# Performance work log

Hardware: AMD Instinct MI355X
Metric: run time of the kernel (lower is better)

Reference implementation:

```python
import jax, jax.numpy as jnp
import numpy as np

B, L, D_MODEL, N_HEADS = 2, 2048, 1024, 16
HEAD_DIM = D_MODEL // N_HEADS  # 64
PAD_START = (3 * L) // 4  # last quarter of keys are padding


def _rope_tables(seq_len, dim, base=10000.0, dtype=jnp.float32):
    inv_freq = 1.0 / (base ** (jnp.arange(0, dim, 2, dtype=jnp.float32) / dim))
    t = jnp.arange(seq_len, dtype=jnp.float32)
    freqs = jnp.einsum('i,j->ij', t, inv_freq)  # (L, dim/2)
    return jnp.cos(freqs).astype(dtype), jnp.sin(freqs).astype(dtype)


def _apply_rope(x, cos, sin):
    # x: (B, H, L, D); cos/sin: (L, D/2)
    cos = cos[None, None]
    sin = sin[None, None]
    x_even, x_odd = x[..., 0::2], x[..., 1::2]
    rot_even = x_even * cos - x_odd * sin
    rot_odd = x_even * sin + x_odd * cos
    return jnp.stack((rot_even, rot_odd), axis=-1).reshape(x.shape)


def setup_inputs() -> dict:
    key = jax.random.key(0)
    k_x, k_wqkv, k_bqkv, k_wout, k_bout = jax.random.split(key, 5)
    x = jax.random.normal(k_x, (B, L, D_MODEL), dtype=jnp.float32)
    Wqkv = jax.random.normal(k_wqkv, (3 * D_MODEL, D_MODEL), dtype=jnp.float32) * 0.02
    bqkv = jax.random.normal(k_bqkv, (3 * D_MODEL,), dtype=jnp.float32) * 0.02
    Wout = jax.random.normal(k_wout, (D_MODEL, D_MODEL), dtype=jnp.float32) * 0.02
    bout = jax.random.normal(k_bout, (D_MODEL,), dtype=jnp.float32) * 0.02
    # True = padded position (end of sequence padded)
    pad_mask = jnp.broadcast_to(jnp.arange(L) >= PAD_START, (B, L))
    return {"x": x, "pad_mask": pad_mask, "Wqkv": Wqkv, "bqkv": bqkv, "Wout": Wout, "bout": bout}


def reference(x, pad_mask, Wqkv, bqkv, Wout, bout):
    Bc, Lc, E = x.shape
    H, D = N_HEADS, HEAD_DIM
    qkv = x @ Wqkv.T + bqkv                       # (B, L, 3E)
    qkv = qkv.reshape(Bc, Lc, 3, H, D)
    q = jnp.transpose(qkv[:, :, 0], (0, 2, 1, 3))  # (B, H, L, D)
    k = jnp.transpose(qkv[:, :, 1], (0, 2, 1, 3))
    v = jnp.transpose(qkv[:, :, 2], (0, 2, 1, 3))
    cos, sin = _rope_tables(Lc, D, dtype=x.dtype)
    q = _apply_rope(q, cos, sin)
    k = _apply_rope(k, cos, sin)
    # Mask exactly as the torch module builds it: attn_mask = causal_upper | key_pad,
    # with torch bool-mask semantics (True = allowed to attend).
    causal_upper = jnp.triu(jnp.ones((Lc, Lc), dtype=bool), 1)[None, None]  # (1,1,L,L)
    key_pad = pad_mask[:, None, None, :]                                     # (B,1,1,L)
    allowed = causal_upper | key_pad                                         # (B,1,L,L)
    scale = 1.0 / jnp.sqrt(jnp.asarray(D, dtype=x.dtype))
    scores = jnp.einsum('bhqd,bhkd->bhqk', q, k) * scale
    scores = jnp.where(allowed, scores, -jnp.inf)
    attn = jax.nn.softmax(scores, axis=-1)
    out = jnp.einsum('bhqk,bhkd->bhqd', attn, v)   # (B, H, L, D)
    out = jnp.transpose(out, (0, 2, 1, 3)).reshape(Bc, Lc, E)
    return out @ Wout.T + bout
```

## Files before the change

kernel.cpp:

```cpp
#include <hip/hip_runtime.h>

#define BB 2
#define LL 2048
#define DM 1024
#define NH 16
#define HD 64
#define PAD_START 1536

typedef short bf16x8 __attribute__((ext_vector_type(8)));
typedef float f32x4 __attribute__((ext_vector_type(4)));

#define MFMA_B16(a, b, c) __builtin_amdgcn_mfma_f32_16x16x32_bf16(a, b, c, 0, 0, 0)

#define GLOAD_LDS16(g, l)                                            \
    __builtin_amdgcn_global_load_lds(                                \
        (const __attribute__((address_space(1))) void*)(g),          \
        (__attribute__((address_space(3))) void*)(l), 16, 0, 0)

__device__ __forceinline__ float bf2f(unsigned short u) {
    union { unsigned int i; float f; } v; v.i = ((unsigned int)u) << 16; return v.f;
}
__device__ __forceinline__ unsigned short f2bf(float f) {
    union { float f; unsigned int i; } v; v.f = f;
    unsigned int x = v.i;
    return (unsigned short)((x + 0x7fffu + ((x >> 16) & 1u)) >> 16);
}

__global__ __launch_bounds__(256) void split_kernel(
    const float* __restrict__ X, const float* __restrict__ Wq,
    const float* __restrict__ Wo,
    unsigned short* __restrict__ Xh,
    unsigned short* __restrict__ Wh,
    unsigned short* __restrict__ Woh,
    float* __restrict__ cosT, float* __restrict__ sinT)
{
    if (blockIdx.x >= 8192) {
        const int idx = (blockIdx.x - 8192) * 256 + threadIdx.x;
        const int l = idx >> 5, pp = idx & 31;
        const float LOG2_1E4 = 13.287712379549449f;
        const float invf = exp2f(-((float)pp) * (LOG2_1E4 / 32.0f));
        const float ang = (float)l * invf;
        float2 cs; cs.x = cosf(ang); cs.y = sinf(ang);
        ((float2*)cosT)[idx] = cs;
        return;
    }
    const size_t e = ((size_t)blockIdx.x * 256 + threadIdx.x) * 4;
    const float* src; unsigned short* dh; size_t o;
    if (e < 4194304)      { src = X;  dh = Xh;  o = e; }
    else if (e < 7340032) { src = Wq; dh = Wh;  o = e - 4194304; }
    else                  { src = Wo; dh = Woh; o = e - 7340032; }
    float4 v = *(const float4*)(src + o);
    ushort4 hv;
    hv.x = f2bf(v.x); hv.y = f2bf(v.y);
    hv.z = f2bf(v.z); hv.w = f2bf(v.w);
    *(ushort4*)(dh + o) = hv;
}

__device__ __forceinline__ void qk_frag(
    f32x4 cf, int r0, int bh, int d, float bv, float qscale,
    const float2* __restrict__ ct2,
    unsigned short* __restrict__ dst, bool odd)
{
    const int p = d >> 1;
#pragma unroll
    for (int e = 0; e < 4; ++e) {
        const int l = (r0 + e) & (LL - 1);
        const float x = cf[e] + bv;
        const float px = __shfl_xor(x, 1);
        const float2 cs = ct2[l * 32 + p];
        const float ve = odd ? px : x;
        const float vo = odd ? x : px;
        float res = odd ? (ve * cs.y + vo * cs.x) : (ve * cs.x - vo * cs.y);
        res *= qscale;
        const float other = __shfl_xor(res, 1);
        if (!odd) {
            const unsigned int pk = ((unsigned int)f2bf(res)) |
                                    (((unsigned int)f2bf(other)) << 16);
            *(unsigned int*)(dst + ((size_t)bh * LL + l) * HD + d) = pk;
        }
    }
}

__device__ __forceinline__ void v_frag(
    f32x4 cf, int l0, int bh, int d, float bv, unsigned short* __restrict__ vt)
{
    ushort4 pk;
    pk.x = f2bf(cf[0] + bv); pk.y = f2bf(cf[1] + bv);
    pk.z = f2bf(cf[2] + bv); pk.w = f2bf(cf[3] + bv);
    *(ushort4*)(vt + ((size_t)(bh * HD + d)) * LL + l0) = pk;
}

__device__ __forceinline__ void out_frag(
    f32x4 cf, int r0, int c, float bv, float* __restrict__ C)
{
#pragma unroll
    for (int e = 0; e < 4; ++e)
        C[(size_t)(r0 + e) * DM + c] = cf[e] + bv;
}

__global__ __launch_bounds__(512) void qkv_mfma(
    const unsigned short* __restrict__ Xh,
    const unsigned short* __restrict__ Wh,
    const float* __restrict__ bias,
    const float* __restrict__ cosT,
    unsigned short* __restrict__ qs, unsigned short* __restrict__ ks,
    unsigned short* __restrict__ vt)
{
    __shared__ unsigned short As[2 * 256 * 64];
    __shared__ unsigned short Bs[2 * 192 * 64];

    const int bid = blockIdx.y * 16 + blockIdx.x;
    const int xcd = bid & 7;
    const int i   = bid >> 3;
    const int mt  = (xcd & 3) * 4 + (i & 3);
    const int nt  = (xcd >> 2) * 8 + (i >> 2);
    const int m0 = mt * 256, n0 = nt * 192;

    const int t = threadIdx.x;
    const int lane = t & 63;
    const int w = t >> 6;
    const int wm = w >> 2;
    const int wn = w & 3;
    const int lm = lane & 15;
    const int quad = lane >> 4;

    const int rop = lane >> 3;
    const int sw  = ((lane & 7) ^ rop) * 8;
    const unsigned short* ga = Xh + (size_t)(m0 + w * 32 + rop) * 1024 + sw;
    const unsigned short* gb = Wh + (size_t)(n0 + w * 24 + rop) * 1024 + sw;
    unsigned short* lA = As + (w * 32) * 64;
    unsigned short* lB = Bs + (w * 24) * 64;

    const int o1 = (quad ^ (lm & 7)) * 8;
    const int o2 = ((quad + 4) ^ (lm & 7)) * 8;
    const int ar = (wm * 128 + lm) * 64;
    const int br = (wn * 48 + lm) * 64;

    f32x4 acc[8][3];
#pragma unroll
    for (int mf = 0; mf < 8; ++mf)
#pragma unroll
        for (int nf = 0; nf < 3; ++nf) acc[mf][nf] = (f32x4){0.f,0.f,0.f,0.f};

#define STG(ABO, BBO, k0)                                                 \
    do {                                                                  \
        GLOAD_LDS16(ga + (k0),             lA + (ABO));                   \
        GLOAD_LDS16(ga + (k0) +  8 * 1024, lA + (ABO) +  8 * 64);         \
        GLOAD_LDS16(ga + (k0) + 16 * 1024, lA + (ABO) + 16 * 64);         \
        GLOAD_LDS16(ga + (k0) + 24 * 1024, lA + (ABO) + 24 * 64);         \
        GLOAD_LDS16(gb + (k0),             lB + (BBO));                   \
        GLOAD_LDS16(gb + (k0) +  8 * 1024, lB + (BBO) +  8 * 64);         \
        GLOAD_LDS16(gb + (k0) + 16 * 1024, lB + (BBO) + 16 * 64);         \
    } while (0)

#define TILE(ABO, BBO, SG, KS, VMN)                                      \
    {                                                                     \
        bf16x8 af[8][2]; bf16x8 bfr[3][2];                                \
        _Pragma("unroll")                                                 \
        for (int mf = 0; mf < 8; ++mf) {                                  \
            af[mf][0] = *(const bf16x8*)(As + (ABO) + ar + mf * 1024 + o1);\
            af[mf][1] = *(const bf16x8*)(As + (ABO) + ar + mf * 1024 + o2);\
        }                                                                 \
        _Pragma("unroll")                                                 \
        for (int nf = 0; nf < 3; ++nf) {                                  \
            bfr[nf][0] = *(const bf16x8*)(Bs + (BBO) + br + nf * 1024 + o1);\
            bfr[nf][1] = *(const bf16x8*)(Bs + (BBO) + br + nf * 1024 + o2);\
        }                                                                 \
        asm volatile("s_waitcnt lgkmcnt(0)" ::: "memory");                \
        __builtin_amdgcn_sched_barrier(0);                                \
        __builtin_amdgcn_s_barrier();                                     \
        if (SG) { STG(ABO, BBO, KS); }      \
        asm volatile("s_waitcnt vmcnt(" VMN ")" ::: "memory");            \
        __builtin_amdgcn_sched_barrier(0);                                \
        __builtin_amdgcn_s_barrier();                                     \
        __builtin_amdgcn_s_setprio(1);                                    \
        _Pragma("unroll")                                                 \
        for (int mf = 0; mf < 8; ++mf) {                                  \
            _Pragma("unroll")                                             \
            for (int nf = 0; nf < 3; ++nf) {                              \
                acc[mf][nf] = MFMA_B16(af[mf][0], bfr[nf][0], acc[mf][nf]);\
                acc[mf][nf] = MFMA_B16(af[mf][1], bfr[nf][1], acc[mf][nf]);\
            }                                                             \
        }                                                                 \
        __builtin_amdgcn_s_setprio(0);                                    \
    }

    STG(0, 0, 0);
    STG(16384, 12288, 64);
    asm volatile("s_waitcnt vmcnt(7)" ::: "memory");
    __builtin_amdgcn_sched_barrier(0);
    __builtin_amdgcn_s_barrier();

    for (int k0 = 0; k0 < 896; k0 += 128) {
        TILE(0,     0,     1, k0 + 128, "7")
        TILE(16384, 12288, 1, k0 + 192, "7")
    }
    TILE(0,     0,     0, 0, "0")
    TILE(16384, 12288, 0, 0, "0")
#undef TILE
#undef STG

    const int bi = m0 >> 11;
    const int rbase = m0 + wm * 128;
    const int cbase = n0 + wn * 48;
    const bool odd = (lm & 1) != 0;
    const float2* ct2 = (const float2*)cosT;

#pragma unroll
    for (int nf = 0; nf < 3; ++nf) {
        const int col0 = cbase + nf * 16;
        const int s = col0 >> 10;
        const int h = (col0 & 1023) >> 6;
        const int bh = bi * NH + h;
        const int d = (col0 & 63) + lm;
        const float bv = bias[col0 + lm];
        if (s == 2) {
#pragma unroll
            for (int mf = 0; mf < 8; ++mf)
                v_frag(acc[mf][nf], (rbase + mf * 16 + quad * 4) & (LL - 1),
                       bh, d, bv, vt);
        } else {
            unsigned short* dst = (s == 0) ? qs : ks;
            const float qscale = (s == 0) ? 0.125f : 1.0f;
#pragma unroll
            for (int mf = 0; mf < 8; ++mf)
                qk_frag(acc[mf][nf], rbase + mf * 16 + quad * 4, bh,
                        d, bv, qscale, ct2, dst, odd);
        }
    }
}

__global__ __launch_bounds__(256) void attn_mfma(
    const unsigned short* __restrict__ qs,
    const unsigned short* __restrict__ ks,
    const unsigned short* __restrict__ vt,
    unsigned short* __restrict__ aoh)
{
    __shared__ unsigned short Ks[2][64 * 72];
    __shared__ unsigned short Vs[2][64 * 72];
    __shared__ unsigned short Pl[4][16 * 72];

    const int bh = blockIdx.y;
    const int qt = (blockIdx.x + blockIdx.y) & 31;
    const int q0 = qt * 64;
    const int b = bh >> 4, h = bh & (NH - 1);
    const int tid = threadIdx.x;
    const int w = tid >> 6;
    const int lane = tid & 63;
    const int lm = lane & 15;
    const int quad = lane >> 4;
    const int qw0 = q0 + w * 16;

    const unsigned short* qbase = qs + ((size_t)bh * LL + qw0 + lm) * HD + quad * 8;
    const bf16x8 qf0 = *(const bf16x8*)(qbase);
    const bf16x8 qf1 = *(const bf16x8*)(qbase + 32);

    f32x4 O[4];
#pragma unroll
    for (int dd = 0; dd < 4; ++dd) O[dd] = (f32x4){0.f, 0.f, 0.f, 0.f};
    float lrow[4] = {0.f, 0.f, 0.f, 0.f};

    const unsigned short* kbase = ks + (size_t)bh * LL * HD;
    const unsigned short* vtb   = vt + (size_t)bh * HD * LL;
    unsigned short* pw = &Pl[w][0];

    const int srow = tid >> 3;
    const int sch  = (tid & 7) * 8;

    const int t0 = ((q0 < PAD_START) ? q0 : PAD_START) >> 6;

    int k0 = t0 * 64;
    uint4 ka0 = *(const uint4*)(kbase + (size_t)(k0 + srow) * HD + sch);
    uint4 ka1 = *(const uint4*)(kbase + (size_t)(k0 + srow + 32) * HD + sch);
    uint4 va0 = *(const uint4*)(vtb + (size_t)srow * LL + k0 + sch);
    uint4 va1 = *(const uint4*)(vtb + (size_t)(srow + 32) * LL + k0 + sch);
    {
        unsigned short* Kc = &Ks[t0 & 1][0];
        unsigned short* Vc = &Vs[t0 & 1][0];
        *(uint4*)(Kc + srow * 72 + sch)        = ka0;
        *(uint4*)(Kc + (srow + 32) * 72 + sch) = ka1;
        *(uint4*)(Vc + srow * 72 + sch)        = va0;
        *(uint4*)(Vc + (srow + 32) * 72 + sch) = va1;
    }
    __syncthreads();

    for (int tt = t0; tt < 32; ++tt) {
        k0 = tt * 64;
        const int cur = tt & 1;
        const unsigned short* Kc = &Ks[cur][0];
        const unsigned short* Vc = &Vs[cur][0];
        unsigned short* Kn = &Ks[cur ^ 1][0];
        unsigned short* Vn = &Vs[cur ^ 1][0];

        {
            const int kn = ((tt + 1) < 32 ? (tt + 1) : 31) * 64;
            ka0 = *(const uint4*)(kbase + (size_t)(kn + srow) * HD + sch);
            ka1 = *(const uint4*)(kbase + (size_t)(kn + srow + 32) * HD + sch);
            va0 = *(const uint4*)(vtb + (size_t)srow * LL + kn + sch);
            va1 = *(const uint4*)(vtb + (size_t)(srow + 32) * LL + kn + sch);
        }

        f32x4 sfrag[4];
#pragma unroll
        for (int c = 0; c < 4; ++c) {
            const bf16x8 kf0 = *(const bf16x8*)(Kc + (c * 16 + lm) * 72 + quad * 8);
            const bf16x8 kf1 = *(const bf16x8*)(Kc + (c * 16 + lm) * 72 + 32 + quad * 8);
            f32x4 z = (f32x4){0.f, 0.f, 0.f, 0.f};
            z = MFMA_B16(qf0, kf0, z);
            z = MFMA_B16(qf1, kf1, z);
            sfrag[c] = z;
        }
        if (tt == t0 && q0 < PAD_START) {
#pragma unroll
            for (int c = 0; c < 4; ++c) {
                const int kg = k0 + c * 16 + lm;
#pragma unroll
                for (int r = 0; r < 4; ++r) {
                    const int qg = qw0 + quad * 4 + r;
                    if (kg <= qg) sfrag[c][r] = -1e30f;
                }
            }
        }
#pragma unroll
        for (int r = 0; r < 4; ++r) {
#pragma unroll
            for (int c = 0; c < 4; ++c) {
                const float p = __expf(sfrag[c][r]);
                lrow[r] += p;
                pw[(quad * 4 + r) * 72 + c * 16 + lm] = f2bf(p);
            }
        }
        const bf16x8 a0 = *(const bf16x8*)(pw + lm * 72 + quad * 8);
        const bf16x8 a1 = *(const bf16x8*)(pw + lm * 72 + 32 + quad * 8);
#pragma unroll
        for (int dd = 0; dd < 4; ++dd) {
            const bf16x8 b0 = *(const bf16x8*)(Vc + (dd * 16 + lm) * 72 + quad * 8);
            const bf16x8 b1 = *(const bf16x8*)(Vc + (dd * 16 + lm) * 72 + 32 + quad * 8);
            O[dd] = MFMA_B16(a0, b0, O[dd]);
            O[dd] = MFMA_B16(a1, b1, O[dd]);
        }

        *(uint4*)(Kn + srow * 72 + sch)        = ka0;
        *(uint4*)(Kn + (srow + 32) * 72 + sch) = ka1;
        *(uint4*)(Vn + srow * 72 + sch)        = va0;
        *(uint4*)(Vn + (srow + 32) * 72 + sch) = va1;
        __syncthreads();
    }

#pragma unroll
    for (int r = 0; r < 4; ++r) {
        float rs = lrow[r];
        rs += __shfl_xor(rs, 1);
        rs += __shfl_xor(rs, 2);
        rs += __shfl_xor(rs, 4);
        rs += __shfl_xor(rs, 8);
        lrow[r] = rs;
    }

#pragma unroll
    for (int r = 0; r < 4; ++r) {
        const float inv = 1.0f / lrow[r];
        const int qg = qw0 + quad * 4 + r;
        const size_t base = ((size_t)(b * LL + qg)) * DM + h * HD;
#pragma unroll
        for (int dd = 0; dd < 4; ++dd)
            aoh[base + dd * 16 + lm] = f2bf(O[dd][r] * inv);
    }
}

__global__ __launch_bounds__(256) void out_mfma(
    const unsigned short* __restrict__ Ah,
    const unsigned short* __restrict__ Wh,
    const float* __restrict__ bias, float* __restrict__ C)
{
    __shared__ unsigned short As[128 * 64];
    __shared__ unsigned short Bs[128 * 64];
    const int n0 = blockIdx.x * 128;
    const int m0 = blockIdx.y * 128;

    f32x4 c00 = {0,0,0,0}, c01 = {0,0,0,0}, c02 = {0,0,0,0}, c03 = {0,0,0,0};
    f32x4 c10 = {0,0,0,0}, c11 = {0,0,0,0}, c12 = {0,0,0,0}, c13 = {0,0,0,0};
    f32x4 c20 = {0,0,0,0}, c21 = {0,0,0,0}, c22 = {0,0,0,0}, c23 = {0,0,0,0};
    f32x4 c30 = {0,0,0,0}, c31 = {0,0,0,0}, c32 = {0,0,0,0}, c33 = {0,0,0,0};

    const int t = threadIdx.x;
    const int lane = t & 63;
    const int w = t >> 6;
    const int wm = (w >> 1) << 6;
    const int wn = (w & 1) << 6;
    const int lm = lane & 15;
    const int quad = lane >> 4;

    const int rop = lane >> 3;
    const int sw  = ((lane & 7) ^ rop) * 8;
    const unsigned short* ga = Ah + (size_t)(m0 + w * 32 + rop) * 1024 + sw;
    const unsigned short* gb = Wh + (size_t)(n0 + w * 32 + rop) * 1024 + sw;
    unsigned short* lA = As + (w * 32) * 64;
    unsigned short* lB = Bs + (w * 32) * 64;

    const int o1 = (quad ^ (lm & 7)) * 8;
    const int o2 = ((quad + 4) ^ (lm & 7)) * 8;
    const int arow = (wm + lm) * 64;
    const int brow = (wn + lm) * 64;

    for (int k0 = 0; k0 < 1024; k0 += 64) {
        __syncthreads();
        GLOAD_LDS16(ga + k0,             lA);
        GLOAD_LDS16(ga + k0 +  8 * 1024, lA +  8 * 64);
        GLOAD_LDS16(ga + k0 + 16 * 1024, lA + 16 * 64);
        GLOAD_LDS16(ga + k0 + 24 * 1024, lA + 24 * 64);
        GLOAD_LDS16(gb + k0,             lB);
        GLOAD_LDS16(gb + k0 +  8 * 1024, lB +  8 * 64);
        GLOAD_LDS16(gb + k0 + 16 * 1024, lB + 16 * 64);
        GLOAD_LDS16(gb + k0 + 24 * 1024, lB + 24 * 64);
        __syncthreads();
        {
            bf16x8 a0 = *(const bf16x8*)(As + arow +  0 * 64 + o1);
            bf16x8 a1 = *(const bf16x8*)(As + arow + 16 * 64 + o1);
            bf16x8 a2 = *(const bf16x8*)(As + arow + 32 * 64 + o1);
            bf16x8 a3 = *(const bf16x8*)(As + arow + 48 * 64 + o1);
            bf16x8 b0 = *(const bf16x8*)(Bs + brow +  0 * 64 + o1);
            bf16x8 b1 = *(const bf16x8*)(Bs + brow + 16 * 64 + o1);
            bf16x8 b2 = *(const bf16x8*)(Bs + brow + 32 * 64 + o1);
            bf16x8 b3 = *(const bf16x8*)(Bs + brow + 48 * 64 + o1);
            c00 = MFMA_B16(a0, b0, c00); c01 = MFMA_B16(a0, b1, c01);
            c02 = MFMA_B16(a0, b2, c02); c03 = MFMA_B16(a0, b3, c03);
            c10 = MFMA_B16(a1, b0, c10); c11 = MFMA_B16(a1, b1, c11);
            c12 = MFMA_B16(a1, b2, c12); c13 = MFMA_B16(a1, b3, c13);
            c20 = MFMA_B16(a2, b0, c20); c21 = MFMA_B16(a2, b1, c21);
            c22 = MFMA_B16(a2, b2, c22); c23 = MFMA_B16(a2, b3, c23);
            c30 = MFMA_B16(a3, b0, c30); c31 = MFMA_B16(a3, b1, c31);
            c32 = MFMA_B16(a3, b2, c32); c33 = MFMA_B16(a3, b3, c33);
        }
        {
            bf16x8 a0 = *(const bf16x8*)(As + arow +  0 * 64 + o2);
            bf16x8 a1 = *(const bf16x8*)(As + arow + 16 * 64 + o2);
            bf16x8 a2 = *(const bf16x8*)(As + arow + 32 * 64 + o2);
            bf16x8 a3 = *(const bf16x8*)(As + arow + 48 * 64 + o2);
            bf16x8 b0 = *(const bf16x8*)(Bs + brow +  0 * 64 + o2);
            bf16x8 b1 = *(const bf16x8*)(Bs + brow + 16 * 64 + o2);
            bf16x8 b2 = *(const bf16x8*)(Bs + brow + 32 * 64 + o2);
            bf16x8 b3 = *(const bf16x8*)(Bs + brow + 48 * 64 + o2);
            c00 = MFMA_B16(a0, b0, c00); c01 = MFMA_B16(a0, b1, c01);
            c02 = MFMA_B16(a0, b2, c02); c03 = MFMA_B16(a0, b3, c03);
            c10 = MFMA_B16(a1, b0, c10); c11 = MFMA_B16(a1, b1, c11);
            c12 = MFMA_B16(a1, b2, c12); c13 = MFMA_B16(a1, b3, c13);
            c20 = MFMA_B16(a2, b0, c20); c21 = MFMA_B16(a2, b1, c21);
            c22 = MFMA_B16(a2, b2, c22); c23 = MFMA_B16(a2, b3, c23);
            c30 = MFMA_B16(a3, b0, c30); c31 = MFMA_B16(a3, b1, c31);
            c32 = MFMA_B16(a3, b2, c32); c33 = MFMA_B16(a3, b3, c33);
        }
    }

#define CSTORE(rt, ct) \
    out_frag(c##rt##ct, m0 + wm + rt * 16 + quad * 4, \
             n0 + wn + ct * 16 + lm, bias[n0 + wn + ct * 16 + lm], C);
    CSTORE(0,0) CSTORE(0,1) CSTORE(0,2) CSTORE(0,3)
    CSTORE(1,0) CSTORE(1,1) CSTORE(1,2) CSTORE(1,3)
    CSTORE(2,0) CSTORE(2,1) CSTORE(2,2) CSTORE(2,3)
    CSTORE(3,0) CSTORE(3,1) CSTORE(3,2) CSTORE(3,3)
#undef CSTORE
}

extern "C" void kernel_launch(void* const* d_in, const int* in_sizes, int n_in,
                              void* d_out, int out_size, void* d_ws, size_t ws_size,
                              hipStream_t stream)
{
    const float* x    = (const float*)d_in[0];
    const float* Wqkv = (const float*)d_in[2];
    const float* bqkv = (const float*)d_in[3];
    const float* Wout = (const float*)d_in[4];
    const float* bout = (const float*)d_in[5];
    float* out = (float*)d_out;

    unsigned short* p = (unsigned short*)d_ws;
    const size_t SZ = (size_t)BB * NH * LL * HD;
    unsigned short* qsb = p; p += SZ;
    unsigned short* ksb = p; p += SZ;
    unsigned short* vtb = p; p += SZ;
    unsigned short* Xhi = p; p += SZ;
    unsigned short* Whi = p; p += (size_t)3145728;
    unsigned short* Wohi = p; p += (size_t)1048576;
    float* cosT = (float*)p; p += (size_t)4 * 65536;

    split_kernel<<<8448, 256, 0, stream>>>(x, Wqkv, Wout,
                                           Xhi, Whi, Wohi, cosT, nullptr);
    dim3 g1(16, 16);
    qkv_mfma<<<g1, 512, 0, stream>>>(Xhi, Whi, bqkv, cosT,
                                     qsb, ksb, vtb);
    dim3 g2(32, 32);
    attn_mfma<<<g2, 256, 0, stream>>>(qsb, ksb, vtb, Xhi);
    dim3 g3(8, 32);
    out_mfma<<<g3, 256, 0, stream>>>(Xhi, Wohi, bout, out);
}
```

Before: 215.3 us.

## Stage attention K/V tiles via direct global-to-LDS loads with XOR swizzle

Replaces register-staged K/V tile loads (global to VGPR, then ds_write) with direct global_load_lds transfers into an unpadded 64-wide LDS layout. An XOR swizzle on the 16-byte chunk index replaces the previous 72-element row padding to avoid bank conflicts. The block index is also remapped so that the blocks for a given batch-head land on the same XCD, which improves L2 reuse of K/V. The main risk is the synchronisation of the async LDS loads: the loop relies only on __syncthreads with no explicit vmcnt wait, and the staging writes a per-wave 512-element contiguous region whose mapping must match the swizzled reads.

```diff
diff --git a/kernel.cpp b/kernel.cpp
--- a/kernel.cpp
+++ b/kernel.cpp
@@ -236,12 +236,15 @@
     const unsigned short* __restrict__ vt,
     unsigned short* __restrict__ aoh)
 {
-    __shared__ unsigned short Ks[2][64 * 72];
-    __shared__ unsigned short Vs[2][64 * 72];
+    __shared__ unsigned short Ks[2][64 * 64];
+    __shared__ unsigned short Vs[2][64 * 64];
     __shared__ unsigned short Pl[4][16 * 72];
 
-    const int bh = blockIdx.y;
-    const int qt = (blockIdx.x + blockIdx.y) & 31;
+    const int bid = blockIdx.y * 32 + blockIdx.x;
+    const int xcd = bid & 7;
+    const int j   = bid >> 3;
+    const int bh  = xcd * 4 + (j & 3);
+    const int qt  = ((j >> 2) + bh) & 31;
     const int q0 = qt * 64;
     const int b = bh >> 4, h = bh & (NH - 1);
     const int tid = threadIdx.x;
@@ -264,47 +267,46 @@
     const unsigned short* vtb   = vt + (size_t)bh * HD * LL;
     unsigned short* pw = &Pl[w][0];
 
-    const int srow = tid >> 3;
-    const int sch  = (tid & 7) * 8;
+    const int rop = lane >> 3;
+    const int sw8 = ((lane & 7) ^ rop) * 8;
+    const int r0 = w * 16 + rop;
+    const int r1 = w * 16 + 8 + rop;
+    const int o1 = (quad ^ (lm & 7)) * 8;
+    const int o2 = ((quad + 4) ^ (lm & 7)) * 8;
+
+#define ASTAGE(BUF, KK)                                                      \
+    do {                                                                     \
+        GLOAD_LDS16(kbase + (size_t)((KK) + r0) * HD + sw8,                  \
+                    &Ks[BUF][0] + (w * 2) * 512);                            \
+        GLOAD_LDS16(kbase + (size_t)((KK) + r1) * HD + sw8,                  \
+                    &Ks[BUF][0] + (w * 2 + 1) * 512);                        \
+        GLOAD_LDS16(vtb + (size_t)r0 * LL + (KK) + sw8,                      \
+                    &Vs[BUF][0] + (w * 2) * 512);                            \
+        GLOAD_LDS16(vtb + (size_t)r1 * LL + (KK) + sw8,                      \
+                    &Vs[BUF][0] + (w * 2 + 1) * 512);                        \
+    } while (0)
 
     const int t0 = ((q0 < PAD_START) ? q0 : PAD_START) >> 6;
 
-    int k0 = t0 * 64;
-    uint4 ka0 = *(const uint4*)(kbase + (size_t)(k0 + srow) * HD + sch);
-    uint4 ka1 = *(const uint4*)(kbase + (size_t)(k0 + srow + 32) * HD + sch);
-    uint4 va0 = *(const uint4*)(vtb + (size_t)srow * LL + k0 + sch);
-    uint4 va1 = *(const uint4*)(vtb + (size_t)(srow + 32) * LL + k0 + sch);
-    {
-        unsigned short* Kc = &Ks[t0 & 1][0];
-        unsigned short* Vc = &Vs[t0 & 1][0];
-        *(uint4*)(Kc + srow * 72 + sch)        = ka0;
-        *(uint4*)(Kc + (srow + 32) * 72 + sch) = ka1;
-        *(uint4*)(Vc + srow * 72 + sch)        = va0;
-        *(uint4*)(Vc + (srow + 32) * 72 + sch) = va1;
-    }
+    ASTAGE(t0 & 1, t0 * 64);
     __syncthreads();
 
     for (int tt = t0; tt < 32; ++tt) {
-        k0 = tt * 64;
+        const int k0 = tt * 64;
         const int cur = tt & 1;
         const unsigned short* Kc = &Ks[cur][0];
         const unsigned short* Vc = &Vs[cur][0];
-        unsigned short* Kn = &Ks[cur ^ 1][0];
-        unsigned short* Vn = &Vs[cur ^ 1][0];
 
         {
             const int kn = ((tt + 1) < 32 ? (tt + 1) : 31) * 64;
-            ka0 = *(const uint4*)(kbase + (size_t)(kn + srow) * HD + sch);
-            ka1 = *(const uint4*)(kbase + (size_t)(kn + srow + 32) * HD + sch);
-            va0 = *(const uint4*)(vtb + (size_t)srow * LL + kn + sch);
-            va1 = *(const uint4*)(vtb + (size_t)(srow + 32) * LL + kn + sch);
+            ASTAGE(cur ^ 1, kn);
         }
 
         f32x4 sfrag[4];
 #pragma unroll
         for (int c = 0; c < 4; ++c) {
-            const bf16x8 kf0 = *(const bf16x8*)(Kc + (c * 16 + lm) * 72 + quad * 8);
-            const bf16x8 kf1 = *(const bf16x8*)(Kc + (c * 16 + lm) * 72 + 32 + quad * 8);
+            const bf16x8 kf0 = *(const bf16x8*)(Kc + (c * 16 + lm) * 64 + o1);
+            const bf16x8 kf1 = *(const bf16x8*)(Kc + (c * 16 + lm) * 64 + o2);
             f32x4 z = (f32x4){0.f, 0.f, 0.f, 0.f};
             z = MFMA_B16(qf0, kf0, z);
             z = MFMA_B16(qf1, kf1, z);
@@ -334,18 +336,15 @@
         const bf16x8 a1 = *(const bf16x8*)(pw + lm * 72 + 32 + quad * 8);
 #pragma unroll
         for (int dd = 0; dd < 4; ++dd) {
-            const bf16x8 b0 = *(const bf16x8*)(Vc + (dd * 16 + lm) * 72 + quad * 8);
-            const bf16x8 b1 = *(const bf16x8*)(Vc + (dd * 16 + lm) * 72 + 32 + quad * 8);
+            const bf16x8 b0 = *(const bf16x8*)(Vc + (dd * 16 + lm) * 64 + o1);
+            const bf16x8 b1 = *(const bf16x8*)(Vc + (dd * 16 + lm) * 64 + o2);
             O[dd] = MFMA_B16(a0, b0, O[dd]);
             O[dd] = MFMA_B16(a1, b1, O[dd]);
         }
 
-        *(uint4*)(Kn + srow * 72 + sch)        = ka0;
-        *(uint4*)(Kn + (srow + 32) * 72 + sch) = ka1;
-        *(uint4*)(Vn + srow * 72 + sch)        = va0;
-        *(uint4*)(Vn + (srow + 32) * 72 + sch) = va1;
         __syncthreads();
     }
+#undef ASTAGE
 
 #pragma unroll
     for (int r = 0; r < 4; ++r) {
```

Result: no change. 216.5 us (+0.5%).
